# Performance work log

Measured on AMD Instinct MI355X. Metric: run time of the kernel, lower is better.

The kernel has to match this reference:

```python
import jax, jax.numpy as jnp
import numpy as np

B, N, IN_DIM, LATENT = 4, 4096, 1024, 128


def setup_inputs() -> dict:
    key = jax.random.key(0)
    ks = jax.random.split(key, 9)
    s_in = 1.0 / np.sqrt(IN_DIM)
    s_lat = 1.0 / np.sqrt(LATENT)
    return {
        "Q": jax.random.normal(ks[0], (B, N, IN_DIM), jnp.float32),
        "K": jax.random.normal(ks[1], (B, N, IN_DIM), jnp.float32),
        "V": jax.random.normal(ks[2], (B, N, IN_DIM), jnp.float32),
        "Wk": jax.random.uniform(ks[3], (LATENT, IN_DIM), jnp.float32, -s_in, s_in),
        "bk": jax.random.uniform(ks[4], (LATENT,), jnp.float32, -s_in, s_in),
        "Wq": jax.random.uniform(ks[5], (LATENT, LATENT), jnp.float32, -s_lat, s_lat),
        "bq": jax.random.uniform(ks[6], (LATENT,), jnp.float32, -s_lat, s_lat),
        "Wv": jax.random.uniform(ks[7], (LATENT, IN_DIM), jnp.float32, -s_in, s_in),
        "bv": jax.random.uniform(ks[8], (LATENT,), jnp.float32, -s_in, s_in),
    }


def reference(Q, K, V, Wk, bk, Wq, bq, Wv, bv):
    # NOTE: faithful to original quirks: input K is ignored; Q is re-projected
    # from key_prj(Q); qry_prj has in_dim == latent_dim for this to typecheck.
    Kp = jnp.einsum('bni,oi->bno', Q, Wk) + bk            # [B,N,LATENT]
    Qp = jnp.einsum('bnl,ol->bno', Kp, Wq) + bq           # [B,N,LATENT]
    Vp = jnp.einsum('bni,oi->bno', V, Wv) + bv            # [B,N,LATENT]
    n = Kp.shape[1]
    # score = bmm(K, Q^T) / sqrt(seq_len)  -> [B, N, N]
    scores = jnp.einsum('bnd,bmd->bnm', Kp, Qp) / jnp.sqrt(jnp.asarray(n, scores_dtype(Kp)))
    W = jax.nn.softmax(scores, axis=-2)                   # softmax over rows (dim=-2)
    # Y = (V^T @ W)^T = W^T @ V -> [B, N, LATENT]
    Y = jnp.einsum('bnm,bnd->bmd', W, Vp)
    return Y


def scores_dtype(x):
    return x.dtype
```

## Files before the change

### kernel.cpp

```cpp
#include <hip/hip_runtime.h>
#include <hip/hip_bf16.h>
#include <math.h>

#define NB     4
#define NTOK   4096
#define IND    1024
#define LAT    128
#define MTOT   (NB*NTOK)
#define L2E    1.4426950408889634f
#define SC2    0.022542110013890053f

typedef short bf16x8 __attribute__((ext_vector_type(8)));
typedef float f32x4  __attribute__((ext_vector_type(4)));
typedef float f32x16 __attribute__((ext_vector_type(16)));

__device__ __forceinline__ unsigned short f2bf(float x) {
    union { float f; unsigned int u; } v; v.f = x;
    unsigned int r = v.u + 0x7FFFu + ((v.u >> 16) & 1u);
    return (unsigned short)(r >> 16);
}
__device__ __forceinline__ float bf2f(unsigned short b) {
    union { unsigned int u; float f; } v; v.u = ((unsigned int)b) << 16;
    return v.f;
}
__device__ __forceinline__ unsigned cvtpk(float lo, float hi) {
    unsigned r;
    asm("v_cvt_pk_bf16_f32 %0, %1, %2" : "=v"(r) : "v"(lo), "v"(hi));
    return r;
}
__device__ __forceinline__ void permswap(unsigned &x, unsigned &y) {
    asm volatile("v_permlane32_swap_b32 %0, %1" : "+v"(x), "+v"(y));
}
__device__ __forceinline__ void gld16(const void* g, void* l) {
    __builtin_amdgcn_global_load_lds(
        (const __attribute__((address_space(1))) void*)g,
        (__attribute__((address_space(3))) void*)l, 16, 0, 0);
}

__global__ __launch_bounds__(256) void fuse_w(const float* __restrict__ Wq,
                                              const float* __restrict__ Wk,
                                              const float* __restrict__ bk,
                                              const float* __restrict__ bq,
                                              unsigned short* __restrict__ Wcomb,
                                              float* __restrict__ bqk) {
    const int o = blockIdx.y;
    const int i = blockIdx.x * 256 + threadIdx.x;
    Wcomb[(size_t)o * IND + i] = f2bf(Wk[(size_t)o * IND + i]);
    float acc = 0.f;
    #pragma unroll 8
    for (int l = 0; l < 128; ++l)
        acc = fmaf(Wq[o * 128 + l], Wk[(size_t)l * IND + i], acc);
    Wcomb[(size_t)(128 + o) * IND + i] = f2bf(acc * SC2);
    if (blockIdx.x == 0 && threadIdx.x == 0) {
        float b = bq[o];
        for (int l = 0; l < 128; ++l) b = fmaf(Wq[o * 128 + l], bk[l], b);
        bqk[o] = b * SC2;
    }
}

__global__ __launch_bounds__(256, 6) void proj_all(const float* __restrict__ Q,
                                                   const unsigned short* __restrict__ Wcomb,
                                                   const float* __restrict__ bk,
                                                   const float* __restrict__ bqk,
                                                   unsigned short* __restrict__ Kp,
                                                   unsigned short* __restrict__ Qp,
                                                   const float* __restrict__ V,
                                                   const float* __restrict__ Wv,
                                                   const float* __restrict__ bv,
                                                   unsigned short* __restrict__ VpT) {
    __shared__ __align__(16) char lds[2048 + 16384];
    const int t = threadIdx.x, l = t & 63, w = t >> 6;
    const int lrow = l & 15, lhi = l >> 4;

    const int ar_row = t >> 3, ar_ch = t & 7;

    if (blockIdx.x < 512) {
        const int br = blockIdx.x;
        const int wr = (w >> 1) * 16, wc = (w & 1) * 128;
        f32x4 acc[8] = {};

        const int br_row = t >> 2, br_ch = t & 3;

        float4 aR;
        bf16x8 bR[4];
        aR = *(const float4*)&Q[(size_t)(br * 32 + ar_row) * IND + ar_ch * 4];
        #pragma unroll
        for (int j = 0; j < 4; ++j) {
            int row = br_row + j * 64;
            bR[j] = *(const bf16x8*)&Wcomb[(size_t)row * IND + br_ch * 8];
        }

        for (int k0 = 0; k0 < IND; k0 += 32) {
            {
                union { unsigned short s[4]; unsigned long long q; } pk;
                pk.s[0] = f2bf(aR.x); pk.s[1] = f2bf(aR.y);
                pk.s[2] = f2bf(aR.z); pk.s[3] = f2bf(aR.w);
                *(unsigned long long*)(lds + ((ar_row * 64 + ar_ch * 8) ^ ((ar_row & 3) << 4))) = pk.q;
            }
            #pragma unroll
            for (int j = 0; j < 4; ++j) {
                int row = br_row + j * 64;
                *(bf16x8*)(lds + 2048 + ((row * 64 + br_ch * 16) ^ ((row & 3) << 4))) = bR[j];
            }
            if (k0 + 32 < IND) {
                aR = *(const float4*)&Q[(size_t)(br * 32 + ar_row) * IND + k0 + 32 + ar_ch * 4];
                #pragma unroll
                for (int j = 0; j < 4; ++j) {
                    int row = br_row + j * 64;
                    bR[j] = *(const bf16x8*)&Wcomb[(size_t)row * IND + k0 + 32 + br_ch * 8];
                }
            }
            __syncthreads();

            const int arow = wr + lrow;
            bf16x8 a = *(const bf16x8*)(lds + ((arow * 64 + lhi * 16) ^ ((arow & 3) << 4)));
            #pragma unroll
            for (int n = 0; n < 8; ++n) {
                const int brow = wc + n * 16 + lrow;
                bf16x8 b = *(const bf16x8*)(lds + 2048 +
                    ((brow * 64 + lhi * 16) ^ ((brow & 3) << 4)));
                acc[n] = __builtin_amdgcn_mfma_f32_16x16x32_bf16(a, b, acc[n], 0, 0, 0);
            }
            __syncthreads();
        }

        const int row0 = br * 32 + wr + lhi * 4;
        unsigned short* out = (wc == 0) ? Kp : Qp;
        const float* bias = (wc == 0) ? bk : bqk;
        #pragma unroll
        for (int n = 0; n < 8; ++n) {
            int col = n * 16 + lrow;
            float bv_ = bias[col];
            #pragma unroll
            for (int r = 0; r < 4; ++r)
                out[(size_t)(row0 + r) * LAT + col] = f2bf(acc[n][r] + bv_);
        }
    } else {
        const int br = blockIdx.x - 512;
        const int wr = (w >> 1) * 16, wc = (w & 1) * 64;
        f32x4 acc[4] = {};

        const int br_row = t >> 3, br_ch = t & 7;

        float4 aR, bR[4];
        aR = *(const float4*)&V[(size_t)(br * 32 + ar_row) * IND + ar_ch * 4];
        #pragma unroll
        for (int j = 0; j < 4; ++j) {
            int row = br_row + j * 32;
            bR[j] = *(const float4*)&Wv[(size_t)row * IND + br_ch * 4];
        }

        for (int k0 = 0; k0 < IND; k0 += 32) {
            {
                union { unsigned short s[4]; unsigned long long q; } pk;
                pk.s[0] = f2bf(aR.x); pk.s[1] = f2bf(aR.y);
                pk.s[2] = f2bf(aR.z); pk.s[3] = f2bf(aR.w);
                *(unsigned long long*)(lds + ((ar_row * 64 + ar_ch * 8) ^ ((ar_row & 3) << 4))) = pk.q;
            }
            #pragma unroll
            for (int j = 0; j < 4; ++j) {
                int row = br_row + j * 32;
                union { unsigned short s[4]; unsigned long long q; } pk;
                pk.s[0] = f2bf(bR[j].x); pk.s[1] = f2bf(bR[j].y);
                pk.s[2] = f2bf(bR[j].z); pk.s[3] = f2bf(bR[j].w);
                *(unsigned long long*)(lds + 2048 + ((row * 64 + br_ch * 8) ^ ((row & 3) << 4))) = pk.q;
            }
            if (k0 + 32 < IND) {
                aR = *(const float4*)&V[(size_t)(br * 32 + ar_row) * IND + k0 + 32 + ar_ch * 4];
                #pragma unroll
                for (int j = 0; j < 4; ++j) {
                    int row = br_row + j * 32;
                    bR[j] = *(const float4*)&Wv[(size_t)row * IND + k0 + 32 + br_ch * 4];
                }
            }
            __syncthreads();

            const int arow = wr + lrow;
            bf16x8 a = *(const bf16x8*)(lds + ((arow * 64 + lhi * 16) ^ ((arow & 3) << 4)));
            #pragma unroll
            for (int n = 0; n < 4; ++n) {
                const int brow = wc + n * 16 + lrow;
                bf16x8 b = *(const bf16x8*)(lds + 2048 +
                    ((brow * 64 + lhi * 16) ^ ((brow & 3) << 4)));
                acc[n] = __builtin_amdgcn_mfma_f32_16x16x32_bf16(a, b, acc[n], 0, 0, 0);
            }
            __syncthreads();
        }

        const int row0 = br * 32 + wr + lhi * 4;
        const int batch = row0 >> 12, tok = row0 & 4095;
        #pragma unroll
        for (int n = 0; n < 4; ++n) {
            int col = wc + n * 16 + lrow;
            float bv_ = bv[col];
            union { unsigned short s[4]; unsigned long long q; } pk;
            #pragma unroll
            for (int r = 0; r < 4; ++r) pk.s[r] = f2bf(acc[n][r] + bv_);
            *(unsigned long long*)&VpT[(size_t)batch * (LAT * NTOK) + (size_t)col * NTOK + tok] = pk.q;
        }
    }
}

template<int NSPLIT>
__global__ __launch_bounds__(256, 2) void attn7(const unsigned short* __restrict__ Qp,
                                                const unsigned short* __restrict__ Kp,
                                                const unsigned short* __restrict__ VpT,
                                                unsigned short* __restrict__ Opart,
                                                float* __restrict__ lsum,
                                                float* __restrict__ Y) {
    __shared__ __align__(16) char ldsK[2][16384];
    __shared__ __align__(16) char ldsV[2][16384];
    const int t = threadIdx.x, l = t & 63, w = t >> 6;
    const int lane31 = l & 31, hi = l >> 5;

    int qt, b, ck;
    if constexpr (NSPLIT > 1) {
        int x = blockIdx.x;
        int glo = x & 7, rest = x >> 3;
        qt = rest & 31;
        int g = glo + 8 * (rest >> 5);
        b = g / NSPLIT; ck = g % NSPLIT;
    } else {
        qt = blockIdx.x & 31; b = blockIdx.x >> 5; ck = 0;
    }
    const size_t base  = (size_t)b * ((size_t)NTOK * LAT);
    const size_t vbase = (size_t)b * ((size_t)LAT * NTOK);
    const int wq = qt * 128 + w * 32;
    const int k_base = ck * (NTOK / NSPLIT);
    const int kts = (NTOK / NSPLIT) / 64;

    const int kc_row = t >> 4, kc_ch = t & 15;
    const int vc_row = t >> 3, vc_ch = t & 7;

    auto STAGE = [&](int bi, int k_lo) {
        #pragma unroll
        for (int j = 0; j < 4; ++j) {
            int row = kc_row + j * 16;
            gld16(&Kp[base + (size_t)(k_lo + row) * LAT + (kc_ch ^ (row & 15)) * 8],
                  &ldsK[bi][j * 4096 + w * 1024]);
        }
        #pragma unroll
        for (int j = 0; j < 4; ++j) {
            int row = vc_row + j * 32;
            gld16(&VpT[vbase + (size_t)row * NTOK + k_lo + (vc_ch ^ (row & 7)) * 8],
                  &ldsV[bi][j * 4096 + w * 1024]);
        }
    };

    bf16x8 qf[8];
    {
        const size_t qrow = base + (size_t)(wq + lane31) * LAT;
        #pragma unroll
        for (int ds = 0; ds < 8; ++ds)
            qf[ds] = *(const bf16x8*)&Qp[qrow + ds * 16 + hi * 8];
    }

    f32x16 OA[4] = {};
    float lrun = 0.f;

    int buf = 0;
    STAGE(0, k_base);
    asm volatile("s_waitcnt vmcnt(0)" ::: "memory");
    __syncthreads();

    for (int kt = 0; kt < kts; ++kt) {
        if (kt + 1 < kts) STAGE(buf ^ 1, k_base + (kt + 1) * 64);
        const char* lK = ldsK[buf];
        const char* lV = ldsV[buf];

        f32x16 SA[2];
        __builtin_amdgcn_s_setprio(1);
        #pragma unroll
        for (int kb = 0; kb < 2; ++kb) {
            f32x16 s = {};
            const int kr = kb * 32 + lane31;
            const int ksw = (kr & 15) << 4;
            #pragma unroll
            for (int ds = 0; ds < 8; ++ds) {
                bf16x8 kf = *(const bf16x8*)(lK + ((kr * 256 + ds * 32 + hi * 16) ^ ksw));
                s = __builtin_amdgcn_mfma_f32_32x32x16_bf16(kf, qf[ds], s, 0, 0, 0);
            }
            SA[kb] = s;
        }
        __builtin_amdgcn_s_setprio(0);

        #pragma unroll
        for (int kb = 0; kb < 2; ++kb) {
            float p[16];
            #pragma unroll
            for (int r = 0; r < 16; ++r) {
                p[r] = exp2f(SA[kb][r]);
                lrun += p[r];
            }
            unsigned a0 = cvtpk(p[0], p[1]),  a1 = cvtpk(p[2], p[3]);
            unsigned a2 = cvtpk(p[4], p[5]),  a3 = cvtpk(p[6], p[7]);
            permswap(a0, a2); permswap(a1, a3);
            unsigned b0 = cvtpk(p[8], p[9]),   b1 = cvtpk(p[10], p[11]);
            unsigned b2 = cvtpk(p[12], p[13]), b3 = cvtpk(p[14], p[15]);
            permswap(b0, b2); permswap(b1, b3);
            union { unsigned u[4]; bf16x8 v; } f0 = {{a0, a1, a2, a3}};
            union { unsigned u[4]; bf16x8 v; } f1 = {{b0, b1, b2, b3}};

            __builtin_amdgcn_s_setprio(1);
            #pragma unroll
            for (int db = 0; db < 4; ++db) {
                const int d = db * 32 + lane31;
                const int vsw = (d & 7) << 4;
                bf16x8 vfA = *(const bf16x8*)(lV + ((d * 128 + (kb * 2 + 0) * 32 + hi * 16) ^ vsw));
                OA[db] = __builtin_amdgcn_mfma_f32_32x32x16_bf16(vfA, f0.v, OA[db], 0, 0, 0);
                bf16x8 vfB = *(const bf16x8*)(lV + ((d * 128 + (kb * 2 + 1) * 32 + hi * 16) ^ vsw));
                OA[db] = __builtin_amdgcn_mfma_f32_32x32x16_bf16(vfB, f1.v, OA[db], 0, 0, 0);
            }
            __builtin_amdgcn_s_setprio(0);
        }

        asm volatile("s_waitcnt vmcnt(0)" ::: "memory");
        __syncthreads();
        buf ^= 1;
    }

    const float ltot = lrun + __shfl_xor(lrun, 32);

    if constexpr (NSPLIT == 1) {
        const float inv = 1.0f / ltot;
        float* dst = &Y[base + (size_t)(wq + lane31) * LAT];
        #pragma unroll
        for (int db = 0; db < 4; ++db)
            #pragma unroll
            for (int g = 0; g < 4; ++g) {
                f32x4 v;
                #pragma unroll
                for (int j = 0; j < 4; ++j) v[j] = OA[db][4 * g + j] * inv;
                *(f32x4*)&dst[db * 32 + 8 * g + 4 * hi] = v;
            }
    } else {
        const size_t prow = (size_t)ck * MTOT + (size_t)b * NTOK + wq + lane31;
        unsigned short* dst = &Opart[prow * LAT];
        #pragma unroll
        for (int db = 0; db < 4; ++db)
            #pragma unroll
            for (int g = 0; g < 4; ++g) {
                union { unsigned short s[4]; unsigned long long q; } pk;
                #pragma unroll
                for (int j = 0; j < 4; ++j) pk.s[j] = f2bf(OA[db][4 * g + j]);
                *(unsigned long long*)&dst[db * 32 + 8 * g + 4 * hi] = pk.q;
            }
        if (l < 32) lsum[prow] = ltot;
    }
}

template<int S>
__global__ __launch_bounds__(256) void merge3(const unsigned short* __restrict__ Opart,
                                              const float* __restrict__ lsum,
                                              float* __restrict__ Y) {
    const int idx = blockIdx.x * 256 + threadIdx.x;
    const int row = idx >> 4, cc = (idx & 15) * 8;
    float L = 0.f;
    #pragma unroll
    for (int c = 0; c < S; ++c) L += lsum[(size_t)c * MTOT + row];
    float acc[8] = {};
    #pragma unroll
    for (int c = 0; c < S; ++c) {
        bf16x8 v = *(const bf16x8*)&Opart[((size_t)c * MTOT + row) * LAT + cc];
        #pragma unroll
        for (int j = 0; j < 8; ++j)
            acc[j] += bf2f((unsigned short)v[j]);
    }
    const float inv = 1.f / L;
    f32x4 o0, o1;
    #pragma unroll
    for (int j = 0; j < 4; ++j) { o0[j] = acc[j] * inv; o1[j] = acc[4 + j] * inv; }
    *(f32x4*)&Y[(size_t)row * LAT + cc] = o0;
    *(f32x4*)&Y[(size_t)row * LAT + cc + 4] = o1;
}

extern "C" void kernel_launch(void* const* d_in, const int* in_sizes, int n_in,
                              void* d_out, int out_size, void* d_ws, size_t ws_size,
                              hipStream_t stream) {
    const float* Q  = (const float*)d_in[0];
    const float* V  = (const float*)d_in[2];
    const float* Wk = (const float*)d_in[3];
    const float* bk = (const float*)d_in[4];
    const float* Wq = (const float*)d_in[5];
    const float* bq = (const float*)d_in[6];
    const float* Wv = (const float*)d_in[7];
    const float* bv = (const float*)d_in[8];
    float* Y = (float*)d_out;

    char* ws = (char*)d_ws;
    unsigned short* Kp    = (unsigned short*)(ws);
    unsigned short* Qp    = (unsigned short*)(ws + (4 << 20));
    unsigned short* VpT   = (unsigned short*)(ws + (8 << 20));
    unsigned short* Wcomb = (unsigned short*)(ws + (12 << 20));
    float*          bqk   = (float*)         (ws + 13107200);
    float*          lsum  = (float*)         (ws + 13107712);
    unsigned short* Opart = (unsigned short*)(ws + 14680064);
    const size_t need4 = 14680064 + (size_t)4 * MTOT * LAT * 2;

    fuse_w<<<dim3(4, 128), 256, 0, stream>>>(Wq, Wk, bk, bq, Wcomb, bqk);
    proj_all<<<dim3(1024), 256, 0, stream>>>(Q, Wcomb, bk, bqk, Kp, Qp, V, Wv, bv, VpT);

    if (ws_size >= need4) {
        attn7<4><<<dim3(32 * NB * 4), 256, 0, stream>>>(Qp, Kp, VpT, Opart, lsum, nullptr);
        merge3<4><<<dim3(MTOT * 16 / 256), 256, 0, stream>>>(Opart, lsum, Y);
    } else {
        attn7<1><<<dim3(32 * NB), 256, 0, stream>>>(Qp, Kp, VpT, nullptr, nullptr, Y);
    }
}
```

Baseline: 112.4 us.

## Replace LDS-tiled projection GEMM with direct-load single-wave MFMA kernel

Replaces the 256-thread, LDS-staged projection kernel with a 64-thread kernel in which each wave computes a 16x128 output tile, loading A from global memory and B fragments straight from global into MFMA registers with no LDS or barriers. Wv is now converted to bf16 in the weight-fusion kernel so the V path reads bf16 weights. Task IDs are interleaved across blocks so neighbouring blocks share the same input rows. This drops the syncthreads and LDS traffic, but the Q and V rows are now re-read by both panels and the weights are re-read from L2 by every wave with less reuse.

Result: slower. 174.1 us (+54.9%).

```diff
diff --git a/kernel.cpp b/kernel.cpp
--- a/kernel.cpp
+++ b/kernel.cpp
@@ -41,11 +41,14 @@
                                               const float* __restrict__ Wk,
                                               const float* __restrict__ bk,
                                               const float* __restrict__ bq,
+                                              const float* __restrict__ Wv,
                                               unsigned short* __restrict__ Wcomb,
-                                              float* __restrict__ bqk) {
+                                              float* __restrict__ bqk,
+                                              unsigned short* __restrict__ Wvb) {
     const int o = blockIdx.y;
     const int i = blockIdx.x * 256 + threadIdx.x;
     Wcomb[(size_t)o * IND + i] = f2bf(Wk[(size_t)o * IND + i]);
+    Wvb[(size_t)o * IND + i]   = f2bf(Wv[(size_t)o * IND + i]);
     float acc = 0.f;
     #pragma unroll 8
     for (int l = 0; l < 128; ++l)
@@ -58,144 +61,69 @@
     }
 }
 
-__global__ __launch_bounds__(256, 6) void proj_all(const float* __restrict__ Q,
-                                                   const unsigned short* __restrict__ Wcomb,
-                                                   const float* __restrict__ bk,
-                                                   const float* __restrict__ bqk,
-                                                   unsigned short* __restrict__ Kp,
-                                                   unsigned short* __restrict__ Qp,
-                                                   const float* __restrict__ V,
-                                                   const float* __restrict__ Wv,
-                                                   const float* __restrict__ bv,
-                                                   unsigned short* __restrict__ VpT) {
-    __shared__ __align__(16) char lds[2048 + 16384];
-    const int t = threadIdx.x, l = t & 63, w = t >> 6;
-    const int lrow = l & 15, lhi = l >> 4;
-
-    const int ar_row = t >> 3, ar_ch = t & 7;
-
-    if (blockIdx.x < 512) {
-        const int br = blockIdx.x;
-        const int wr = (w >> 1) * 16, wc = (w & 1) * 128;
-        f32x4 acc[8] = {};
-
-        const int br_row = t >> 2, br_ch = t & 3;
-
-        float4 aR;
-        bf16x8 bR[4];
-        aR = *(const float4*)&Q[(size_t)(br * 32 + ar_row) * IND + ar_ch * 4];
-        #pragma unroll
-        for (int j = 0; j < 4; ++j) {
-            int row = br_row + j * 64;
-            bR[j] = *(const bf16x8*)&Wcomb[(size_t)row * IND + br_ch * 8];
-        }
-
-        for (int k0 = 0; k0 < IND; k0 += 32) {
-            {
-                union { unsigned short s[4]; unsigned long long q; } pk;
-                pk.s[0] = f2bf(aR.x); pk.s[1] = f2bf(aR.y);
-                pk.s[2] = f2bf(aR.z); pk.s[3] = f2bf(aR.w);
-                *(unsigned long long*)(lds + ((ar_row * 64 + ar_ch * 8) ^ ((ar_row & 3) << 4))) = pk.q;
-            }
-            #pragma unroll
-            for (int j = 0; j < 4; ++j) {
-                int row = br_row + j * 64;
-                *(bf16x8*)(lds + 2048 + ((row * 64 + br_ch * 16) ^ ((row & 3) << 4))) = bR[j];
-            }
-            if (k0 + 32 < IND) {
-                aR = *(const float4*)&Q[(size_t)(br * 32 + ar_row) * IND + k0 + 32 + ar_ch * 4];
-                #pragma unroll
-                for (int j = 0; j < 4; ++j) {
-                    int row = br_row + j * 64;
-                    bR[j] = *(const bf16x8*)&Wcomb[(size_t)row * IND + k0 + 32 + br_ch * 8];
-                }
-            }
-            __syncthreads();
-
-            const int arow = wr + lrow;
-            bf16x8 a = *(const bf16x8*)(lds + ((arow * 64 + lhi * 16) ^ ((arow & 3) << 4)));
-            #pragma unroll
-            for (int n = 0; n < 8; ++n) {
-                const int brow = wc + n * 16 + lrow;
-                bf16x8 b = *(const bf16x8*)(lds + 2048 +
-                    ((brow * 64 + lhi * 16) ^ ((brow & 3) << 4)));
-                acc[n] = __builtin_amdgcn_mfma_f32_16x16x32_bf16(a, b, acc[n], 0, 0, 0);
-            }
-            __syncthreads();
-        }
-
-        const int row0 = br * 32 + wr + lhi * 4;
-        unsigned short* out = (wc == 0) ? Kp : Qp;
-        const float* bias = (wc == 0) ? bk : bqk;
+__global__ __launch_bounds__(64) void proj_direct(const float* __restrict__ Q,
+                                                  const unsigned short* __restrict__ Wcomb,
+                                                  const float* __restrict__ bk,
+                                                  const float* __restrict__ bqk,
+                                                  unsigned short* __restrict__ Kp,
+                                                  unsigned short* __restrict__ Qp,
+                                                  const float* __restrict__ V,
+                                                  const unsigned short* __restrict__ Wvb,
+                                                  const float* __restrict__ bv,
+                                                  unsigned short* __restrict__ VpT) {
+    const int task = (blockIdx.x >> 3) + (blockIdx.x & 7) * 384;
+    const int l = threadIdx.x, lrow = l & 15, lhi = l >> 4;
+
+    const float* A;
+    const unsigned short* B;
+    int rt, panel;
+    if (task < 2048) {
+        rt = task >> 1; panel = task & 1;
+        A = Q + (size_t)(rt * 16 + lrow) * IND;
+        B = Wcomb + (size_t)panel * 128 * IND;
+    } else {
+        rt = task - 2048; panel = -1;
+        A = V + (size_t)(rt * 16 + lrow) * IND;
+        B = Wvb;
+    }
+
+    f32x4 acc[8] = {};
+
+    #pragma unroll 2
+    for (int k0 = 0; k0 < IND; k0 += 32) {
+        float4 a0 = *(const float4*)&A[k0 + lhi * 8];
+        float4 a1 = *(const float4*)&A[k0 + lhi * 8 + 4];
+        union { unsigned u[4]; bf16x8 v; } af;
+        af.u[0] = cvtpk(a0.x, a0.y); af.u[1] = cvtpk(a0.z, a0.w);
+        af.u[2] = cvtpk(a1.x, a1.y); af.u[3] = cvtpk(a1.z, a1.w);
         #pragma unroll
         for (int n = 0; n < 8; ++n) {
-            int col = n * 16 + lrow;
-            float bv_ = bias[col];
-            #pragma unroll
-            for (int r = 0; r < 4; ++r)
-                out[(size_t)(row0 + r) * LAT + col] = f2bf(acc[n][r] + bv_);
-        }
-    } else {
-        const int br = blockIdx.x - 512;
-        const int wr = (w >> 1) * 16, wc = (w & 1) * 64;
-        f32x4 acc[4] = {};
-
-        const int br_row = t >> 3, br_ch = t & 7;
-
-        float4 aR, bR[4];
-        aR = *(const float4*)&V[(size_t)(br * 32 + ar_row) * IND + ar_ch * 4];
-        #pragma unroll
-        for (int j = 0; j < 4; ++j) {
-            int row = br_row + j * 32;
-            bR[j] = *(const float4*)&Wv[(size_t)row * IND + br_ch * 4];
-        }
-
-        for (int k0 = 0; k0 < IND; k0 += 32) {
-            {
-                union { unsigned short s[4]; unsigned long long q; } pk;
-                pk.s[0] = f2bf(aR.x); pk.s[1] = f2bf(aR.y);
-                pk.s[2] = f2bf(aR.z); pk.s[3] = f2bf(aR.w);
-                *(unsigned long long*)(lds + ((ar_row * 64 + ar_ch * 8) ^ ((ar_row & 3) << 4))) = pk.q;
-            }
-            #pragma unroll
-            for (int j = 0; j < 4; ++j) {
-                int row = br_row + j * 32;
-                union { unsigned short s[4]; unsigned long long q; } pk;
-                pk.s[0] = f2bf(bR[j].x); pk.s[1] = f2bf(bR[j].y);
-                pk.s[2] = f2bf(bR[j].z); pk.s[3] = f2bf(bR[j].w);
-                *(unsigned long long*)(lds + 2048 + ((row * 64 + br_ch * 8) ^ ((row & 3) << 4))) = pk.q;
-            }
-            if (k0 + 32 < IND) {
-                aR = *(const float4*)&V[(size_t)(br * 32 + ar_row) * IND + k0 + 32 + ar_ch * 4];
-                #pragma unroll
-                for (int j = 0; j < 4; ++j) {
-                    int row = br_row + j * 32;
-                    bR[j] = *(const float4*)&Wv[(size_t)row * IND + k0 + 32 + br_ch * 4];
-                }
-            }
-            __syncthreads();
-
-            const int arow = wr + lrow;
-            bf16x8 a = *(const bf16x8*)(lds + ((arow * 64 + lhi * 16) ^ ((arow & 3) << 4)));
-            #pragma unroll
-            for (int n = 0; n < 4; ++n) {
-                const int brow = wc + n * 16 + lrow;
-                bf16x8 b = *(const bf16x8*)(lds + 2048 +
-                    ((brow * 64 + lhi * 16) ^ ((brow & 3) << 4)));
-                acc[n] = __builtin_amdgcn_mfma_f32_16x16x32_bf16(a, b, acc[n], 0, 0, 0);
-            }
-            __syncthreads();
-        }
-
-        const int row0 = br * 32 + wr + lhi * 4;
+            bf16x8 bf = *(const bf16x8*)&B[(size_t)(n * 16 + lrow) * IND + k0 + lhi * 8];
+            acc[n] = __builtin_amdgcn_mfma_f32_16x16x32_bf16(af.v, bf, acc[n], 0, 0, 0);
+        }
+    }
+
+    const int row0 = rt * 16 + lhi * 4;
+    if (panel >= 0) {
+        unsigned short* out = (panel == 0) ? Kp : Qp;
+        const float* bias = (panel == 0) ? bk : bqk;
+        #pragma unroll
+        for (int n = 0; n < 8; ++n) {
+            const int col = n * 16 + lrow;
+            const float bv_ = bias[col];
+            #pragma unroll
+            for (int j = 0; j < 4; ++j)
+                out[(size_t)(row0 + j) * LAT + col] = f2bf(acc[n][j] + bv_);
+        }
+    } else {
         const int batch = row0 >> 12, tok = row0 & 4095;
         #pragma unroll
-        for (int n = 0; n < 4; ++n) {
-            int col = wc + n * 16 + lrow;
-            float bv_ = bv[col];
+        for (int n = 0; n < 8; ++n) {
+            const int col = n * 16 + lrow;
+            const float bv_ = bv[col];
             union { unsigned short s[4]; unsigned long long q; } pk;
             #pragma unroll
-            for (int r = 0; r < 4; ++r) pk.s[r] = f2bf(acc[n][r] + bv_);
+            for (int j = 0; j < 4; ++j) pk.s[j] = f2bf(acc[n][j] + bv_);
             *(unsigned long long*)&VpT[(size_t)batch * (LAT * NTOK) + (size_t)col * NTOK + tok] = pk.q;
         }
     }
@@ -394,11 +322,12 @@
     unsigned short* Wcomb = (unsigned short*)(ws + (12 << 20));
     float*          bqk   = (float*)         (ws + 13107200);
     float*          lsum  = (float*)         (ws + 13107712);
+    unsigned short* Wvb   = (unsigned short*)(ws + 13369856);
     unsigned short* Opart = (unsigned short*)(ws + 14680064);
     const size_t need4 = 14680064 + (size_t)4 * MTOT * LAT * 2;
 
-    fuse_w<<<dim3(4, 128), 256, 0, stream>>>(Wq, Wk, bk, bq, Wcomb, bqk);
-    proj_all<<<dim3(1024), 256, 0, stream>>>(Q, Wcomb, bk, bqk, Kp, Qp, V, Wv, bv, VpT);
+    fuse_w<<<dim3(4, 128), 256, 0, stream>>>(Wq, Wk, bk, bq, Wv, Wcomb, bqk, Wvb);
+    proj_direct<<<dim3(3072), 64, 0, stream>>>(Q, Wcomb, bk, bqk, Kp, Qp, V, Wvb, bv, VpT);
 
     if (ws_size >= need4) {
         attn7<4><<<dim3(32 * NB * 4), 256, 0, stream>>>(Qp, Kp, VpT, Opart, lsum, nullptr);
```
